# Kernel optimization log

Measured on AMD Instinct MI355X. Metric: run time of the kernel, lower is better.

The kernel has to match this reference:

```python
import jax, jax.numpy as jnp
import numpy as np
import math

N_NODES = 2000
LOOKBACK = 24
IN_DIM = 16
EMB_DIM = 64
BATCH = 32
LN_EPS = 1e-5


def _layernorm(v, g, b):
    mu = jnp.mean(v, axis=-1, keepdims=True)
    var = jnp.var(v, axis=-1, keepdims=True)
    return (v - mu) * jax.lax.rsqrt(var + LN_EPS) * g + b


def setup_inputs() -> dict:
    key = jax.random.key(0)
    ks = jax.random.split(key, 12)
    td = LOOKBACK * IN_DIM  # 384
    s_in = 1.0 / math.sqrt(td)
    s_d = 1.0 / math.sqrt(IN_DIM)
    return {
        "x": jax.random.normal(ks[0], (BATCH, N_NODES, LOOKBACK, IN_DIM), jnp.float32),
        "Wq": jax.random.normal(ks[1], (td, EMB_DIM), jnp.float32) * s_in,
        "bq": jax.random.normal(ks[2], (EMB_DIM,), jnp.float32) * 0.01,
        "Wk": jax.random.normal(ks[3], (td, EMB_DIM), jnp.float32) * s_in,
        "bk": jax.random.normal(ks[4], (EMB_DIM,), jnp.float32) * 0.01,
        "g0": jnp.ones((EMB_DIM,), jnp.float32),
        "beta0": jnp.zeros((EMB_DIM,), jnp.float32),
        "g1": jnp.ones((EMB_DIM,), jnp.float32),
        "beta1": jnp.zeros((EMB_DIM,), jnp.float32),
        "normal": jax.random.normal(ks[5], (N_NODES, LOOKBACK, IN_DIM), jnp.float32),
        "Win": jax.random.normal(ks[6], (IN_DIM, IN_DIM), jnp.float32) * s_d,
    }


def reference(x, Wq, bq, Wk, bk, g0, beta0, g1, beta1, normal, Win):
    b, n, t, d = x.shape
    xf = x.reshape(b, n, t * d)
    # per-sample q/k linear + layernorm (batched over b)
    q1 = _layernorm(xf @ Wq + bq, g0, beta0)  # (b, n, e)
    k1 = _layernorm(xf @ Wk + bk, g1, beta1)  # (b, n, e)
    # node-mixing attention: softmax(q k^T / sqrt(num_nodes)) @ normal
    scores = jnp.einsum('bne,bme->bnm', q1, k1) / math.sqrt(n)
    A = jax.nn.softmax(scores, axis=-1)  # (b, n, n)
    data = jnp.einsum('bnm,mf->bnf', A, normal.reshape(n, t * d)).reshape(b, n, t, d)
    # RPPsAtt attention weights over time (general attention, output_len = 1)
    query = x[:, :, -1, :] @ Win  # (b, n, d)
    att = jnp.einsum('bnd,bntd->bnt', query, data)  # scores vs context
    weight = jax.nn.softmax(att, axis=-1)  # (b, n, t)
    # res = stack(weights).permute(0,1,3,2) -> (b, n, t, 1), broadcast-add
    return data + weight[..., None]
```

## Files before the change

kernel.cpp:

```cpp
#include <hip/hip_runtime.h>
#include <math.h>

#define B_   32
#define NN   2000
#define NP   2048
#define TT   24
#define TD   384
#define EE   64
#define SCALE 0.022360679774997896f
#define S2E   0.032259642f
#define CLP   43.28f

typedef __bf16 bf16;
typedef __bf16 bf16x8 __attribute__((ext_vector_type(8)));
typedef float  f32x4  __attribute__((ext_vector_type(4)));

typedef __attribute__((address_space(3))) unsigned int       lds_u32;
typedef const __attribute__((address_space(1))) unsigned int g_u32;

__device__ __forceinline__ void dma16(const void* g, void* l) {
    __builtin_amdgcn_global_load_lds((g_u32*)g, (lds_u32*)l, 16, 0, 0);
}

__device__ __forceinline__ bool input_is_bf16(const void* g0) {
    return *reinterpret_cast<const unsigned short*>(g0) == 0x3F80;
}

__device__ __forceinline__ float safexp(float v) {
    return __expf(fminf(fmaxf(v, -30.f), 30.f));
}

__device__ __forceinline__ bf16x8 ld_frag(const bf16* p) {
    return *reinterpret_cast<const bf16x8*>(p);
}

__device__ __forceinline__ bf16x8 cvt8_f32(const float* p) {
    f32x4 a = *reinterpret_cast<const f32x4*>(p);
    f32x4 b = *reinterpret_cast<const f32x4*>(p + 4);
    bf16x8 r;
    r[0]=(bf16)a[0]; r[1]=(bf16)a[1]; r[2]=(bf16)a[2]; r[3]=(bf16)a[3];
    r[4]=(bf16)b[0]; r[5]=(bf16)b[1]; r[6]=(bf16)b[2]; r[7]=(bf16)b[3];
    return r;
}

__global__ __launch_bounds__(256) void prep_k(
        const void* Wqv, const void* Wkv, bf16* __restrict__ Wp,
        const void* normalv, bf16* __restrict__ Vp,
        const void* xv, const void* Winv, float* __restrict__ Qry,
        const void* gflag) {
    bool bfl = input_is_bf16(gflag);
    int bid = blockIdx.x;
    if (bid < 192) {
        int o = bid*256 + threadIdx.x;
        int j  = o & 7;
        int l  = (o >> 3) & 63;
        int nt = (o >> 9) & 7;
        int ks = o >> 12;
        int k   = ks*32 + ((l >> 4) * 8) + j;
        int col = nt*16 + (l & 15);
        float v;
        if (bfl) v = (col < 64) ? (float)((const bf16*)Wqv)[k*64 + col]
                                : (float)((const bf16*)Wkv)[k*64 + col - 64];
        else     v = (col < 64) ? ((const float*)Wqv)[k*64 + col]
                                : ((const float*)Wkv)[k*64 + col - 64];
        Wp[o] = (bf16)v;
    } else if (bid < 3264) {
        int o = (bid - 192)*256 + threadIdx.x;
        int j  = o & 7;
        int l  = (o >> 3) & 63;
        int nt = (o >> 9) % 24;
        int kb = o / (24*512);
        int key = kb*32 + ((l >> 4) * 8) + j;
        int col = nt*16 + (l & 15);
        float v = 0.f;
        if (key < NN)
            v = bfl ? (float)((const bf16*)normalv)[key*TD + col]
                    : ((const float*)normalv)[key*TD + col];
        Vp[o] = (bf16)v;
    } else {
        int o = (bid - 3264)*256 + threadIdx.x;
        int d2 = o & 15;
        int n  = (o >> 4) & (NP - 1);
        int b  = o >> 15;
        float acc = 0.f;
        if (n < NN) {
            size_t xoff = ((size_t)(b*NN + n))*TD + (TT-1)*16;
            if (bfl) {
                const bf16* xr = (const bf16*)xv + xoff;
                const bf16* Wn = (const bf16*)Winv;
                #pragma unroll
                for (int d = 0; d < 16; ++d) acc += (float)xr[d] * (float)Wn[d*16 + d2];
            } else {
                const float* xr = (const float*)xv + xoff;
                const float* Wn = (const float*)Winv;
                #pragma unroll
                for (int d = 0; d < 16; ++d) acc += xr[d] * Wn[d*16 + d2];
            }
        }
        Qry[o] = acc;
    }
}

__global__ __launch_bounds__(256) void proj_ln_k(
        const void* xv, const bf16* __restrict__ Wp,
        const void* bqv, const void* bkv,
        const void* g0v, const void* be0v,
        const void* g1v, const void* be1v,
        bf16* __restrict__ Qb, bf16* __restrict__ Kp) {
    __shared__ __align__(16) bf16 Wbuf[2][4096];
    bool bf = input_is_bf16(g0v);
    int mb = blockIdx.x, b = blockIdx.y;
    int w    = threadIdx.x >> 6;
    int lane = threadIdx.x & 63;
    int quad = lane >> 4, lq = lane & 15;

    int rowA = mb*64 + w*16 + lq;
    int xrow = rowA < NN ? rowA : NN - 1;

    bf16x8 afr[12];
    if (bf) {
        const bf16* xp = (const bf16*)xv + ((size_t)(b*NN + xrow))*TD + quad*8;
        #pragma unroll
        for (int ks = 0; ks < 12; ++ks) afr[ks] = ld_frag(xp + ks*32);
    } else {
        const float* xp = (const float*)xv + ((size_t)(b*NN + xrow))*TD + quad*8;
        #pragma unroll
        for (int ks = 0; ks < 12; ++ks) afr[ks] = cvt8_f32(xp + ks*32);
    }

    auto stage = [&](int ks, int bufi) {
        const char* g = (const char*)Wp + (size_t)ks*8192;
        for (int c = w; c < 8; c += 4)
            dma16(g + c*1024 + (size_t)lane*16, &Wbuf[bufi][c*512]);
    };
    stage(0, 0);

    f32x4 acc[8];
    #pragma unroll
    for (int nt = 0; nt < 8; ++nt) acc[nt] = (f32x4){0.f, 0.f, 0.f, 0.f};
    __syncthreads();

    for (int ks = 0; ks < 12; ++ks) {
        int cur = ks & 1;
        if (ks + 1 < 12) stage(ks + 1, cur ^ 1);
        const bf16* wb = Wbuf[cur];
        #pragma unroll
        for (int nt = 0; nt < 8; ++nt) {
            bf16x8 bfr = ld_frag(wb + nt*512 + lane*8);
            acc[nt] = __builtin_amdgcn_mfma_f32_16x16x32_bf16(afr[ks], bfr, acc[nt], 0, 0, 0);
        }
        __syncthreads();
    }

    #pragma unroll
    for (int nt = 0; nt < 8; ++nt) {
        int c = nt*16 + lq;
        float bias;
        if (bf) bias = (c < 64) ? (float)((const bf16*)bqv)[c] : (float)((const bf16*)bkv)[c-64];
        else    bias = (c < 64) ? ((const float*)bqv)[c] : ((const float*)bkv)[c-64];
        #pragma unroll
        for (int r = 0; r < 4; ++r) acc[nt][r] += bias;
    }
    float outn[8][4];
    #pragma unroll
    for (int g = 0; g < 2; ++g) {
        float s[4], sq[4];
        #pragma unroll
        for (int r = 0; r < 4; ++r) {
            float p = 0.f, p2 = 0.f;
            #pragma unroll
            for (int nt = 0; nt < 4; ++nt) {
                float v = acc[g*4 + nt][r];
                p += v; p2 += v*v;
            }
            s[r] = p; sq[r] = p2;
        }
        #pragma unroll
        for (int m = 1; m < 16; m <<= 1) {
            #pragma unroll
            for (int r = 0; r < 4; ++r) {
                s[r]  += __shfl_xor(s[r],  m, 16);
                sq[r] += __shfl_xor(sq[r], m, 16);
            }
        }
        #pragma unroll
        for (int r = 0; r < 4; ++r) {
            float mean = s[r] * (1.f/64.f);
            float var  = fmaxf(sq[r] * (1.f/64.f) - mean*mean, 0.f);
            float rs   = rsqrtf(var + 1e-5f);
            #pragma unroll
            for (int nt = 0; nt < 4; ++nt) {
                int c = nt*16 + lq;
                float gv, bv;
                if (g == 0) { gv = bf ? (float)((const bf16*)g0v)[c] : ((const float*)g0v)[c];
                              bv = bf ? (float)((const bf16*)be0v)[c] : ((const float*)be0v)[c]; }
                else        { gv = bf ? (float)((const bf16*)g1v)[c] : ((const float*)g1v)[c];
                              bv = bf ? (float)((const bf16*)be1v)[c] : ((const float*)be1v)[c]; }
                outn[g*4 + nt][r] = (acc[g*4 + nt][r] - mean) * rs * gv + bv;
            }
        }
    }
    int rowq = mb*64 + w*16 + quad*4;
    #pragma unroll
    for (int r = 0; r < 4; ++r) {
        int row = rowq + r;
        bool real = row < NN;
        size_t qbase = ((size_t)(b*NP + row))*EE;
        int kb2  = row >> 5;
        int half = (row >> 4) & 1;
        int lqk  = row & 15;
        #pragma unroll
        for (int nt = 0; nt < 4; ++nt) {
            Qb[qbase + nt*16 + lq] = (bf16)(real ? outn[nt][r] : 0.f);
            int col   = nt*16 + lq;
            int f     = half*2 + (col >> 5);
            int quadk = (col >> 3) & 3;
            size_t idx = (((size_t)(b*64 + kb2)*4 + f)*64 + quadk*16 + lqk)*8 + (col & 7);
            Kp[idx] = (bf16)(real ? outn[4 + nt][r] : 0.f);
        }
    }
}

__global__ __launch_bounds__(512, 4) void attn_k(
        const bf16* __restrict__ Qb, const bf16* __restrict__ Kp,
        const bf16* __restrict__ Vp, const float* __restrict__ Qry,
        void* outv, const void* gflag) {
    __shared__ __align__(16) char SM[49920];
    bf16*  PlB   = (bf16*)(SM);
    bf16*  scr   = (bf16*)(SM + 16384);
    float* eBuf  = (float*)(SM + 42496);
    float* denP  = (float*)(SM + 49152);
    float* dnInv = (float*)(SM + 49664);

    bool bf = input_is_bf16(gflag);
    int mb = blockIdx.x, b = blockIdx.y;
    int w    = threadIdx.x >> 6;
    int lane = threadIdx.x & 63;
    int quad = lane >> 4, lq = lane & 15;
    int rowbase = mb*64;
    int rt = w >> 1;
    int h  = w & 1;

    const bf16* qp = Qb + ((size_t)(b*NP + rowbase + rt*16 + lq))*EE + quad*8;
    bf16x8 aq0 = ld_frag(qp);
    bf16x8 aq1 = ld_frag(qp + 32);

    f32x4 acc[4][3];
    #pragma unroll
    for (int i = 0; i < 4; ++i)
        #pragma unroll
        for (int ct = 0; ct < 3; ++ct) acc[i][ct] = (f32x4){0.f, 0.f, 0.f, 0.f};
    float den[4] = {0.f, 0.f, 0.f, 0.f};

    const bf16* kbase = Kp + (size_t)(b*64)*2048;
    const int koff = h*1024 + lane*8;
    const int voff = w*1536 + lane*8;

    const int pb = (h*2 + (lq >> 3))*128 + quad*32 + (lq & 7);

    auto barrier_p = [&]() {
        asm volatile("s_waitcnt lgkmcnt(0)" ::: "memory");
        __builtin_amdgcn_s_barrier();
        __builtin_amdgcn_sched_barrier(0);
    };
    auto ldK = [&](int kb, bf16x8& k0, bf16x8& k1) {
        const bf16* p = kbase + kb*2048 + koff;
        k0 = ld_frag(p);
        k1 = ld_frag(p + 512);
    };
    auto ldV = [&](int kb, bf16x8& v0, bf16x8& v1, bf16x8& v2) {
        const bf16* p = Vp + kb*12288 + voff;
        v0 = ld_frag(p);
        v1 = ld_frag(p + 512);
        v2 = ld_frag(p + 1024);
    };
    auto qk_emit = [&](bf16x8 k0, bf16x8 k1, int slot, bool maskpad) {
        f32x4 s = (f32x4){0.f,0.f,0.f,0.f};
        s = __builtin_amdgcn_mfma_f32_16x16x32_bf16(aq0, k0, s, 0, 0, 0);
        s = __builtin_amdgcn_mfma_f32_16x16x32_bf16(aq1, k1, s, 0, 0, 0);
        bf16* pw = PlB + slot*2048 + rt*512;
        #pragma unroll
        for (int r = 0; r < 4; ++r) {
            float e = exp2f(fminf(fmaxf(s[r]*S2E, -CLP), CLP));
            if (!maskpad || h == 0) den[r] += e;
            pw[pb + r*8] = (bf16)e;
        }
    };
    auto pv = [&](int slot, bf16x8 v0, bf16x8 v1, bf16x8 v2) {
        const bf16* pl = PlB + slot*2048;
        __builtin_amdgcn_s_setprio(1);
        #pragma unroll
        for (int rt2 = 0; rt2 < 4; ++rt2) {
            bf16x8 ap = ld_frag(pl + rt2*512 + lane*8);
            acc[rt2][0] = __builtin_amdgcn_mfma_f32_16x16x32_bf16(ap, v0, acc[rt2][0], 0, 0, 0);
            acc[rt2][1] = __builtin_amdgcn_mfma_f32_16x16x32_bf16(ap, v1, acc[rt2][1], 0, 0, 0);
            acc[rt2][2] = __builtin_amdgcn_mfma_f32_16x16x32_bf16(ap, v2, acc[rt2][2], 0, 0, 0);
        }
        __builtin_amdgcn_s_setprio(0);
    };

    bf16x8 kA0, kA1, kB0, kB1;
    bf16x8 vA0, vA1, vA2, vB0, vB1, vB2;

    ldK(0, kA0, kA1);
    ldK(1, kB0, kB1);
    ldV(0, vA0, vA1, vA2);
    ldV(1, vB0, vB1, vB2);
    qk_emit(kA0, kA1, 0, false);
    qk_emit(kB0, kB1, 1, false);
    ldK(2, kA0, kA1);
    ldK(3, kB0, kB1);
    barrier_p();

    for (int t = 1; t <= 30; ++t) {
        int E = 2*t;
        int sE = E & 3, sO = (E+1) & 3, sEm2 = (E-2) & 3, sOm2 = (E-1) & 3;
        pv(sEm2, vA0, vA1, vA2);
        ldV(E, vA0, vA1, vA2);
        qk_emit(kA0, kA1, sE, false);
        ldK(E+2, kA0, kA1);
        pv(sOm2, vB0, vB1, vB2);
        ldV(E+1, vB0, vB1, vB2);
        qk_emit(kB0, kB1, sO, false);
        ldK(E+3, kB0, kB1);
        barrier_p();
    }

    pv(0, vA0, vA1, vA2);
    ldV(62, vA0, vA1, vA2);
    qk_emit(kA0, kA1, 2, true);
    pv(1, vB0, vB1, vB2);
    barrier_p();
    pv(2, vA0, vA1, vA2);

    #pragma unroll
    for (int r = 0; r < 4; ++r) {
        float s = den[r];
        s += __shfl_xor(s, 1, 16); s += __shfl_xor(s, 2, 16);
        s += __shfl_xor(s, 4, 16); s += __shfl_xor(s, 8, 16);
        den[r] = s;
    }
    if (lq == 0) {
        #pragma unroll
        for (int r = 0; r < 4; ++r) denP[h*64 + rt*16 + quad*4 + r] = den[r];
    }
    __syncthreads();

    const float* qryb = Qry + ((size_t)(b*NP + rowbase))*16 + lq;
    #pragma unroll
    for (int rt2 = 0; rt2 < 4; ++rt2) {
        float inv[4], qd[4];
        #pragma unroll
        for (int r = 0; r < 4; ++r) {
            int row = rt2*16 + quad*4 + r;
            inv[r] = 1.f / fmaxf(denP[row] + denP[64 + row], 1e-30f);
            qd[r]  = qryb[(size_t)row*16];
        }
        #pragma unroll
        for (int ct = 0; ct < 3; ++ct) {
            #pragma unroll
            for (int r = 0; r < 4; ++r) {
                float v = acc[rt2][ct][r] * inv[r];
                acc[rt2][ct][r] = v;
                float a = v * qd[r];
                a += __shfl_xor(a, 1, 16); a += __shfl_xor(a, 2, 16);
                a += __shfl_xor(a, 4, 16); a += __shfl_xor(a, 8, 16);
                float e = safexp(a);
                if (lq == 0) eBuf[(rt2*16 + quad*4 + r)*26 + (w*3 + ct)] = e;
            }
        }
    }
    __syncthreads();

    if (lane < 8) {
        int row = w*8 + lane;
        float s = 0.f;
        #pragma unroll
        for (int t = 0; t < 24; ++t) s += eBuf[row*26 + t];
        dnInv[row] = 1.f / fmaxf(s, 1e-30f);
    }
    __syncthreads();

    if (bf) {
        #pragma unroll
        for (int half = 0; half < 2; ++half) {
            #pragma unroll
            for (int rti = 0; rti < 2; ++rti) {
                int rt2 = half*2 + rti;
                #pragma unroll
                for (int ct = 0; ct < 3; ++ct) {
                    int t = w*3 + ct;
                    #pragma unroll
                    for (int r = 0; r < 4; ++r) {
                        int row = rt2*16 + quad*4 + r;
                        float wv = eBuf[row*26 + t] * dnInv[row];
                        scr[(size_t)(row - half*32)*408 + t*16 + lq] =
                            (bf16)(acc[rt2][ct][r] + wv);
                    }
                }
            }
            __syncthreads();
            bf16* og = (bf16*)outv + ((size_t)b*NN + rowbase + half*32)*TD;
            #pragma unroll
            for (int i = 0; i < 4; ++i) {
                int lrow = w*4 + i;
                int grow = rowbase + half*32 + lrow;
                if (grow < NN && lane < 48)
                    *reinterpret_cast<bf16x8*>(og + (size_t)lrow*TD + lane*8) =
                        *reinterpret_cast<const bf16x8*>(scr + (size_t)lrow*408 + lane*8);
            }
            __syncthreads();
        }
    } else {
        #pragma unroll
        for (int rt2 = 0; rt2 < 4; ++rt2) {
            #pragma unroll
            for (int ct = 0; ct < 3; ++ct) {
                int t = w*3 + ct;
                #pragma unroll
                for (int r = 0; r < 4; ++r) {
                    int row  = rt2*16 + quad*4 + r;
                    int grow = rowbase + row;
                    if (grow < NN) {
                        float wv = eBuf[row*26 + t] * dnInv[row];
                        ((float*)outv)[((size_t)(b*NN + grow))*TD + t*16 + lq] =
                            acc[rt2][ct][r] + wv;
                    }
                }
            }
        }
    }
}

extern "C" void kernel_launch(void* const* d_in, const int* in_sizes, int n_in,
                              void* d_out, int out_size, void* d_ws, size_t ws_size,
                              hipStream_t stream) {
    const void* x      = d_in[0];
    const void* Wq     = d_in[1];
    const void* bq     = d_in[2];
    const void* Wk     = d_in[3];
    const void* bk     = d_in[4];
    const void* g0     = d_in[5];
    const void* be0    = d_in[6];
    const void* g1     = d_in[7];
    const void* be1    = d_in[8];
    const void* normal = d_in[9];
    const void* Win    = d_in[10];

    char* ws = (char*)d_ws;
    bf16*  Qb  = (bf16*)(ws);
    bf16*  Kp  = (bf16*)(ws + 8388608);
    bf16*  Vp  = (bf16*)(ws + 16777216);
    bf16*  Wp  = (bf16*)(ws + 16777216 + 1638400);
    float* Qry = (float*)(ws + 16777216 + 1638400 + 98304);

    prep_k<<<dim3(7360), dim3(256), 0, stream>>>(Wq, Wk, Wp, normal, Vp, x, Win, Qry, g0);
    proj_ln_k<<<dim3(32, 32), dim3(256), 0, stream>>>(x, Wp, bq, bk, g0, be0, g1, be1, Qb, Kp);
    attn_k<<<dim3(32, 32), dim3(512), 0, stream>>>(Qb, Kp, Vp, Qry, d_out, g0);
}
```

Baseline: 340.2 us.

## Double P-tile ring in LDS to halve barriers in attention main loop

Grows the LDS probability buffer from four to eight slots, which shifts the scratch and reduction buffers. The main loop now processes four K/V tiles per barrier instead of two, running seven unrolled iterations with two barrier phases each. The aim is to cut the number of workgroup barriers and give the QK and PV MFMA stages more room to overlap. The cost is about 16 KB more LDS per block (66 KB against 50 KB), which may lower the number of resident blocks per CU below the launch bound of 4.

Measured after the change: 474.2 us. 1.39x slower.

```diff
diff --git a/kernel.cpp b/kernel.cpp
--- a/kernel.cpp
+++ b/kernel.cpp
@@ -225,12 +225,12 @@
         const bf16* __restrict__ Qb, const bf16* __restrict__ Kp,
         const bf16* __restrict__ Vp, const float* __restrict__ Qry,
         void* outv, const void* gflag) {
-    __shared__ __align__(16) char SM[49920];
+    __shared__ __align__(16) char SM[66304];
     bf16*  PlB   = (bf16*)(SM);
-    bf16*  scr   = (bf16*)(SM + 16384);
-    float* eBuf  = (float*)(SM + 42496);
-    float* denP  = (float*)(SM + 49152);
-    float* dnInv = (float*)(SM + 49664);
+    bf16*  scr   = (bf16*)(SM + 32768);
+    float* eBuf  = (float*)(SM + 58880);
+    float* denP  = (float*)(SM + 65536);
+    float* dnInv = (float*)(SM + 66048);
 
     bool bf = input_is_bf16(gflag);
     int mb = blockIdx.x, b = blockIdx.y;
@@ -306,32 +306,45 @@
     ldK(1, kB0, kB1);
     ldV(0, vA0, vA1, vA2);
     ldV(1, vB0, vB1, vB2);
-    qk_emit(kA0, kA1, 0, false);
-    qk_emit(kB0, kB1, 1, false);
-    ldK(2, kA0, kA1);
-    ldK(3, kB0, kB1);
+    qk_emit(kA0, kA1, 0, false);  ldK(2, kA0, kA1);
+    qk_emit(kB0, kB1, 1, false);  ldK(3, kB0, kB1);
+    qk_emit(kA0, kA1, 2, false);  ldK(4, kA0, kA1);
+    qk_emit(kB0, kB1, 3, false);  ldK(5, kB0, kB1);
     barrier_p();
 
-    for (int t = 1; t <= 30; ++t) {
-        int E = 2*t;
-        int sE = E & 3, sO = (E+1) & 3, sEm2 = (E-2) & 3, sOm2 = (E-1) & 3;
-        pv(sEm2, vA0, vA1, vA2);
-        ldV(E, vA0, vA1, vA2);
-        qk_emit(kA0, kA1, sE, false);
-        ldK(E+2, kA0, kA1);
-        pv(sOm2, vB0, vB1, vB2);
-        ldV(E+1, vB0, vB1, vB2);
-        qk_emit(kB0, kB1, sO, false);
-        ldK(E+3, kB0, kB1);
+    for (int u = 0; u < 7; ++u) {
+        int i0 = 8*u + 4;
+        pv(0, vA0, vA1, vA2);  ldV(i0-2, vA0, vA1, vA2);
+        qk_emit(kA0, kA1, 4, false);  ldK(i0+2, kA0, kA1);
+        pv(1, vB0, vB1, vB2);  ldV(i0-1, vB0, vB1, vB2);
+        qk_emit(kB0, kB1, 5, false);  ldK(i0+3, kB0, kB1);
+        pv(2, vA0, vA1, vA2);  ldV(i0+0, vA0, vA1, vA2);
+        qk_emit(kA0, kA1, 6, false);  ldK(i0+4, kA0, kA1);
+        pv(3, vB0, vB1, vB2);  ldV(i0+1, vB0, vB1, vB2);
+        qk_emit(kB0, kB1, 7, false);  ldK(i0+5, kB0, kB1);
         barrier_p();
-    }
-
-    pv(0, vA0, vA1, vA2);
-    ldV(62, vA0, vA1, vA2);
-    qk_emit(kA0, kA1, 2, true);
-    pv(1, vB0, vB1, vB2);
+        pv(4, vA0, vA1, vA2);  ldV(i0+2, vA0, vA1, vA2);
+        qk_emit(kA0, kA1, 0, false);  ldK(i0+6, kA0, kA1);
+        pv(5, vB0, vB1, vB2);  ldV(i0+3, vB0, vB1, vB2);
+        qk_emit(kB0, kB1, 1, false);  ldK(i0+7, kB0, kB1);
+        pv(6, vA0, vA1, vA2);  ldV(i0+4, vA0, vA1, vA2);
+        qk_emit(kA0, kA1, 2, false);  ldK(i0+8, kA0, kA1);
+        pv(7, vB0, vB1, vB2);  ldV(i0+5, vB0, vB1, vB2);
+        qk_emit(kB0, kB1, 3, false);  ldK(i0+9, kB0, kB1);
+        barrier_p();
+    }
+
+    pv(0, vA0, vA1, vA2);  ldV(58, vA0, vA1, vA2);
+    qk_emit(kA0, kA1, 4, false);  ldK(62, kA0, kA1);
+    pv(1, vB0, vB1, vB2);  ldV(59, vB0, vB1, vB2);
+    qk_emit(kB0, kB1, 5, false);
+    pv(2, vA0, vA1, vA2);  ldV(60, vA0, vA1, vA2);
+    qk_emit(kA0, kA1, 6, true);
     barrier_p();
-    pv(2, vA0, vA1, vA2);
+    pv(3, vB0, vB1, vB2);  ldV(61, vB0, vB1, vB2);
+    pv(4, vA0, vA1, vA2);  ldV(62, vA0, vA1, vA2);
+    pv(5, vB0, vB1, vB2);
+    pv(6, vA0, vA1, vA2);
 
     #pragma unroll
     for (int r = 0; r < 4; ++r) {
```
